# Performance work log

Measured on AMD Instinct MI355X. Metric: run time of the kernel, lower is better.

Reference implementation:

```python
import jax, jax.numpy as jnp
import numpy as np

E = 1024   # embed_dim
H = 16     # num_heads
D = E // H # head_dim
B = 2
S = 2048
YAT_EPS = 0.1


def setup_inputs() -> dict:
    key = jax.random.key(0)
    ks = jax.random.split(key, 5)
    w_scale = (6.0 / (E + E)) ** 0.5  # xavier_uniform bound
    def xavier(k):
        return jax.random.uniform(k, (E, E), jnp.float32, -w_scale, w_scale)
    return {
        "x": jax.random.normal(ks[0], (B, S, E), jnp.float32),
        "Wq": xavier(ks[1]), "bq": jnp.zeros((E,), jnp.float32),
        "Wk": xavier(ks[2]), "bk": jnp.zeros((E,), jnp.float32),
        "Wv": xavier(ks[3]), "bv": jnp.zeros((E,), jnp.float32),
        "Wo": xavier(ks[4]), "bo": jnp.zeros((E,), jnp.float32),
    }


def reference(x, Wq, bq, Wk, bk, Wv, bv, Wo, bo):
    b, s, _ = x.shape
    # Projections (Linear: x @ W + b, flax kernel layout [in, out])
    Q = x @ Wq + bq
    K = x @ Wk + bk
    V = x @ Wv + bv
    # [B, H, S, D]
    Q = Q.reshape(b, s, H, D).transpose(0, 2, 1, 3)
    K = K.reshape(b, s, H, D).transpose(0, 2, 1, 3)
    V = V.reshape(b, s, H, D).transpose(0, 2, 1, 3)
    # L2 normalize along head_dim
    Qn = Q / (jnp.linalg.norm(Q, axis=-1, keepdims=True) + 1e-8)
    Kn = K / (jnp.linalg.norm(K, axis=-1, keepdims=True) + 1e-8)
    # Yat kernel scores: (1 + <q,k>)^2 / (eps + (1 - <q,k>))
    dot = jnp.einsum("bhqd,bhkd->bhqk", Qn, Kn)
    scores = (1.0 + dot) ** 2 / (YAT_EPS + (1.0 - dot))
    # Sum-normalize (no softmax)
    attn = scores / (jnp.sum(scores, axis=-1, keepdims=True) + 1e-6)
    out = jnp.einsum("bhqk,bhkd->bhqd", attn, V)
    out = out.transpose(0, 2, 1, 3).reshape(b, s, E)
    return out @ Wo + bo
```

## Files before the change

### kernel.cpp

```cpp
#include <hip/hip_runtime.h>
#include <math.h>

#define EDIM 1024
#define NH   16
#define HD   64
#define BATCH 2
#define SEQ  2048
#define NROW (BATCH*SEQ)
#define YAT_EPS 0.1f

typedef _Float16 f16;
typedef _Float16 f16x8 __attribute__((ext_vector_type(8)));
typedef _Float16 f16x4 __attribute__((ext_vector_type(4)));
typedef __fp16   h16x2 __attribute__((ext_vector_type(2)));
typedef float    f32x4 __attribute__((ext_vector_type(4)));
typedef float    f32x2 __attribute__((ext_vector_type(2)));

static __device__ __forceinline__ int pk2(float a, float b) {
    union { h16x2 h; int i; } u;
    u.h = __builtin_amdgcn_cvt_pkrtz(a, b);
    return u.i;
}

static __device__ __forceinline__ f32x2 pk_fma(f32x2 a, f32x2 b, f32x2 c) {
    f32x2 d;
    asm("v_pk_fma_f32 %0, %1, %2, %3" : "=v"(d) : "v"(a), "v"(b), "v"(c));
    return d;
}
static __device__ __forceinline__ f32x2 pk_add(f32x2 a, f32x2 b) {
    f32x2 d;
    asm("v_pk_add_f32 %0, %1, %2" : "=v"(d) : "v"(a), "v"(b));
    return d;
}

__global__ __launch_bounds__(256)
void prep_kernel(const float* __restrict__ x, f16* __restrict__ xb,
                 const float* __restrict__ W0, const float* __restrict__ W1,
                 const float* __restrict__ W2, const float* __restrict__ W3,
                 f16* __restrict__ T0, f16* __restrict__ T1,
                 f16* __restrict__ T2, f16* __restrict__ T3)
{
    const int z = blockIdx.z;
    if (z == 4) {
        const int bid = blockIdx.y * 32 + blockIdx.x;
#pragma unroll
        for (int i = 0; i < 4; ++i) {
            const int off = bid * 4096 + i * 1024 + threadIdx.x * 4;
            const float4 v = *(const float4*)(x + off);
            union { int i2[2]; f16x4 h; } o;
            o.i2[0] = pk2(v.x, v.y);
            o.i2[1] = pk2(v.z, v.w);
            *(f16x4*)(xb + off) = o.h;
        }
        return;
    }
    const float* W = (z == 0) ? W0 : (z == 1) ? W1 : (z == 2) ? W2 : W3;
    f16*         Wt = (z == 0) ? T0 : (z == 1) ? T1 : (z == 2) ? T2 : T3;

    __shared__ float T[32][33];
    const int t = threadIdx.x;
    const int r = t >> 3, c4 = (t & 7) * 4;
    const int bi = blockIdx.x * 32, bj = blockIdx.y * 32;
    const float4 v = *(const float4*)(W + (size_t)(bi + r) * 1024 + bj + c4);
    T[r][c4 + 0] = v.x; T[r][c4 + 1] = v.y; T[r][c4 + 2] = v.z; T[r][c4 + 3] = v.w;
    __syncthreads();
    f16x4 o = {(f16)T[c4 + 0][r], (f16)T[c4 + 1][r], (f16)T[c4 + 2][r], (f16)T[c4 + 3][r]};
    *(f16x4*)(Wt + (size_t)(bj + r) * 1024 + bi + c4) = o;
}

template<int BM, int BN, int WM>
__global__ __launch_bounds__(WM * 128, 3)
void gemm_f16(const f16* __restrict__ A,
              const f16* __restrict__ B0, const f16* __restrict__ B1, const f16* __restrict__ B2,
              const float* __restrict__ bi0, const float* __restrict__ bi1, const float* __restrict__ bi2,
              void* __restrict__ o0, void* __restrict__ o1, void* __restrict__ o2,
              int e0, int e1, int e2)
{
    constexpr int NT    = WM * 128;
    constexpr int SR    = NT / 4;
    constexpr int ASL   = BM / SR;
    constexpr int BSL   = BN / SR;
    constexpr int ABUF  = BM * 32;
    constexpr int BBUF  = BN * 32;
    constexpr int WROWS = BM / WM;
    constexpr int MT    = WROWS / 16;
    constexpr int HALVES = BN / 128;
    constexpr int SCH    = 2048 / NT;
    __shared__ __align__(16) char lds[2 * (ABUF + BBUF) * 2];
    f16* As = (f16*)lds;
    f16* Bs = (f16*)lds + 2 * ABUF;

    const int z = blockIdx.z;
    const f16*   Bt   = (z == 0) ? B0  : (z == 1) ? B1  : B2;
    const float* bias = (z == 0) ? bi0 : (z == 1) ? bi1 : bi2;
    void*        Cout = (z == 0) ? o0  : (z == 1) ? o1  : o2;
    const int    epi  = (z == 0) ? e0  : (z == 1) ? e1  : e2;

    const int tid  = threadIdx.x;
    const int lane = tid & 63;
    const int w    = tid >> 6;
    const int cl   = lane & 15;
    const int quad = lane >> 4;
    const int wm = w % WM, wn = w / WM;
    const int bm = blockIdx.x * BM, bn = blockIdx.y * BN;
    const int wmoff = wm * WROWS;

    const int srow = tid >> 2;
    const int sc   = tid & 3;
    const int ssw  = (sc ^ (srow & 3)) * 8;
    const f16* gA = A  + (size_t)(bm + srow) * 1024 + sc * 8;
    const f16* gB = Bt + (size_t)(bn + srow) * 1024 + sc * 8;
    int lAo[ASL], lBo[BSL];
#pragma unroll
    for (int i = 0; i < ASL; ++i) lAo[i] = (srow + i * SR) * 32 + ssw;
#pragma unroll
    for (int i = 0; i < BSL; ++i) lBo[i] = (srow + i * SR) * 32 + ssw;

    f32x4 acc[MT][4];
#pragma unroll
    for (int i = 0; i < MT; ++i)
#pragma unroll
        for (int j = 0; j < 4; ++j) acc[i][j] = (f32x4){0.f, 0.f, 0.f, 0.f};

    f16x8 ra[ASL], rb[BSL];

#pragma unroll
    for (int i = 0; i < ASL; ++i) ra[i] = *(const f16x8*)(gA + (size_t)i * SR * 1024);
#pragma unroll
    for (int i = 0; i < BSL; ++i) rb[i] = *(const f16x8*)(gB + (size_t)i * SR * 1024);
#pragma unroll
    for (int i = 0; i < ASL; ++i) *(f16x8*)(As + lAo[i]) = ra[i];
#pragma unroll
    for (int i = 0; i < BSL; ++i) *(f16x8*)(Bs + lBo[i]) = rb[i];
#pragma unroll
    for (int i = 0; i < ASL; ++i) ra[i] = *(const f16x8*)(gA + (size_t)i * SR * 1024 + 32);
#pragma unroll
    for (int i = 0; i < BSL; ++i) rb[i] = *(const f16x8*)(gB + (size_t)i * SR * 1024 + 32);
    __syncthreads();

    const int fsw = (quad ^ (cl & 3)) * 8;

    for (int it = 0; it < 32; ++it) {
        const int buf = it & 1, nb = buf ^ 1;
        if (it < 31) {
#pragma unroll
            for (int i = 0; i < ASL; ++i) *(f16x8*)(As + nb * ABUF + lAo[i]) = ra[i];
#pragma unroll
            for (int i = 0; i < BSL; ++i) *(f16x8*)(Bs + nb * BBUF + lBo[i]) = rb[i];
        }
        if (it < 30) {
            const int kn = (it + 2) * 32;
#pragma unroll
            for (int i = 0; i < ASL; ++i) ra[i] = *(const f16x8*)(gA + (size_t)i * SR * 1024 + kn);
#pragma unroll
            for (int i = 0; i < BSL; ++i) rb[i] = *(const f16x8*)(gB + (size_t)i * SR * 1024 + kn);
        }
        f16x8 af[MT], bf[4];
#pragma unroll
        for (int mt = 0; mt < MT; ++mt)
            af[mt] = *(const f16x8*)(&As[buf * ABUF + (wmoff + mt * 16 + cl) * 32 + fsw]);
#pragma unroll
        for (int nt = 0; nt < 4; ++nt)
            bf[nt] = *(const f16x8*)(&Bs[buf * BBUF + (wn * 64 + nt * 16 + cl) * 32 + fsw]);
#pragma unroll
        for (int mt = 0; mt < MT; ++mt)
#pragma unroll
            for (int nt = 0; nt < 4; ++nt)
                acc[mt][nt] = __builtin_amdgcn_mfma_f32_16x16x32_f16(af[mt], bf[nt], acc[mt][nt], 0, 0, 0);
        __syncthreads();
    }

    float bcol[4];
#pragma unroll
    for (int nt = 0; nt < 4; ++nt) bcol[nt] = bias[bn + wn * 64 + nt * 16 + cl];
#pragma unroll
    for (int mt = 0; mt < MT; ++mt)
#pragma unroll
        for (int nt = 0; nt < 4; ++nt)
#pragma unroll
            for (int rg = 0; rg < 4; ++rg) acc[mt][nt][rg] += bcol[nt];

    const int b_idx = bm >> 11, sl0 = bm & (SEQ - 1), h0 = bn >> 6;

    if (epi == 0) {
        float* C = (float*)Cout;
#pragma unroll
        for (int mt = 0; mt < MT; ++mt)
#pragma unroll
            for (int rg = 0; rg < 4; ++rg) {
                const int row = bm + wmoff + mt * 16 + quad * 4 + rg;
#pragma unroll
                for (int nt = 0; nt < 4; ++nt)
                    C[(size_t)row * EDIM + bn + wn * 64 + nt * 16 + cl] = acc[mt][nt][rg];
            }
    } else if (epi == 1) {
        if constexpr (BM == 128) {
        f16* C = (f16*)Cout;
        f16* S = (f16*)lds;
#pragma unroll
        for (int h = 0; h < HALVES; ++h) {
            __syncthreads();
            if ((wn >> 1) == h) {
#pragma unroll
                for (int mt = 0; mt < MT; ++mt)
#pragma unroll
                    for (int rg = 0; rg < 4; ++rg) {
                        float ss = 0.f;
#pragma unroll
                        for (int nt = 0; nt < 4; ++nt) ss += acc[mt][nt][rg] * acc[mt][nt][rg];
                        ss += __shfl_xor(ss, 1); ss += __shfl_xor(ss, 2);
                        ss += __shfl_xor(ss, 4); ss += __shfl_xor(ss, 8);
                        const float inv = 1.0f / (sqrtf(ss) + 1e-8f);
                        const int row = wmoff + mt * 16 + quad * 4 + rg;
#pragma unroll
                        for (int nt = 0; nt < 4; ++nt) {
                            const int colh = (wn & 1) * 64 + nt * 16 + cl;
                            S[row * 128 + (((colh >> 3) ^ (row & 15)) * 8) + (colh & 7)] =
                                (f16)(acc[mt][nt][rg] * inv);
                        }
                    }
            }
            __syncthreads();
#pragma unroll
            for (int i = 0; i < SCH; ++i) {
                const int c = tid + i * NT;
                const int s = c >> 4, gi = c & 15;
                f16x8 v = *(const f16x8*)(&S[s * 128 + ((gi ^ (s & 15)) * 8)]);
                const int head = h0 + h * 2 + (gi >> 3), d8 = (gi & 7) * 8;
                *(f16x8*)(C + ((size_t)(b_idx * NH + head) * SEQ + sl0 + s) * HD + d8) = v;
            }
        }
        }
    } else {
        if constexpr (BM == 128) {
        f16* C = (f16*)Cout;
        f16* S = (f16*)lds;
#pragma unroll
        for (int h = 0; h < HALVES; ++h) {
            __syncthreads();
            if ((wn >> 1) == h) {
#pragma unroll
                for (int mt = 0; mt < MT; ++mt) {
                    const int s0 = wmoff + mt * 16 + quad * 4;
#pragma unroll
                    for (int nt = 0; nt < 4; ++nt) {
                        const int colh = (wn & 1) * 64 + nt * 16 + cl;
                        f16x4 o = {(f16)acc[mt][nt][0], (f16)acc[mt][nt][1],
                                   (f16)acc[mt][nt][2], (f16)acc[mt][nt][3]};
                        *(f16x4*)(&S[colh * 128 + (((s0 >> 3) ^ (colh & 15)) * 8) + (s0 & 7)]) = o;
                    }
                }
            }
            __syncthreads();
#pragma unroll
            for (int i = 0; i < SCH; ++i) {
                const int c = tid + i * NT;
                const int colh = c >> 4, gi = c & 15;
                f16x8 v = *(const f16x8*)(&S[colh * 128 + ((gi ^ (colh & 15)) * 8)]);
                const int head = h0 + h * 2 + (colh >> 6), d = colh & 63;
                *(f16x8*)(C + ((size_t)(b_idx * NH + head) * HD + d) * SEQ + sl0 + gi * 8) = v;
            }
        }
        }
    }
}

__global__ __launch_bounds__(512, 4)
void yat_attn(const f16* __restrict__ Qh, const f16* __restrict__ Kh,
              const f16* __restrict__ Vt, f16* __restrict__ AO)
{
    __shared__ __align__(16) char lds[49152];
    f16* Qs = (f16*)lds;
    f16* KB = (f16*)(lds + 16384);
    f16* VB = (f16*)(lds + 32768);

    const int tid  = threadIdx.x;
    const int lane = tid & 63;
    const int w    = tid >> 6;
    const int cl   = lane & 15;
    const int quad = lane >> 4;
    const int wm = w & 3;
    const int wk = w >> 2;
    const int q0 = blockIdx.x * 128;
    const int bh = blockIdx.y;

    const f16* Qg = Qh + (size_t)bh * SEQ * HD;
    const f16* Kg = Kh + (size_t)bh * SEQ * HD;
    const f16* Vg = Vt + (size_t)bh * HD * SEQ;

    const int rkv = tid >> 3;
    const int gkv = tid & 7;
    const f16* gK = Kg + (size_t)rkv * HD + gkv * 8;
    const f16* gV = Vg + (size_t)rkv * SEQ + gkv * 8;
    const int lkOff = rkv * 64 + ((gkv ^ (rkv & 7)) * 8);

    f16x8 kr = *(const f16x8*)(gK);
    f16x8 vr = *(const f16x8*)(gV);

#pragma unroll
    for (int i = 0; i < 2; ++i) {
        const int s0 = tid + i * 512;
        const int row = s0 >> 3, g = s0 & 7;
        f16x8 v = *(const f16x8*)(Qg + (size_t)(q0 + row) * HD + g * 8);
        *(f16x8*)(&Qs[row * 64 + ((g ^ (row & 7)) * 8)]) = v;
    }
    __syncthreads();
    f16x8 qf[2][2];
#pragma unroll
    for (int qt = 0; qt < 2; ++qt)
#pragma unroll
        for (int kb = 0; kb < 2; ++kb)
            qf[qt][kb] = *(const f16x8*)(&Qs[(wm * 32 + qt * 16 + cl) * 64 +
                                             ((kb * 4 + quad) ^ (cl & 7)) * 8]);

    f32x4 O[2][4];
    f32x2 rs_pk[2];
#pragma unroll
    for (int i = 0; i < 2; ++i) {
        rs_pk[i] = (f32x2){0.f, 0.f};
#pragma unroll
        for (int j = 0; j < 4; ++j) O[i][j] = (f32x4){0.f, 0.f, 0.f, 0.f};
    }

    const f32x2 c_m1  = {-1.0f, -1.0f};
    const f32x2 c_u0  = {1.0f + YAT_EPS, 1.0f + YAT_EPS};
    const f32x2 c_m42 = {-4.2f, -4.2f};
    const f32x2 c_441 = {4.41f, 4.41f};

    for (int t = 0; t < 32; ++t) {
        const int buf = t & 1;
        *(f16x8*)(&KB[buf * 4096 + lkOff]) = kr;
        *(f16x8*)(&VB[buf * 4096 + lkOff]) = vr;
        if (t < 31) {
            kr = *(const f16x8*)(gK + (size_t)(t + 1) * 64 * HD);
            vr = *(const f16x8*)(gV + (t + 1) * 64);
        }
        __syncthreads();

        const f16* Ks = KB + buf * 4096;
        const f16* Vs = VB + buf * 4096;

        f32x4 s[2][2];
#pragma unroll
        for (int kt = 0; kt < 2; ++kt)
#pragma unroll
            for (int qt = 0; qt < 2; ++qt) s[kt][qt] = (f32x4){0.f, 0.f, 0.f, 0.f};
        __builtin_amdgcn_s_setprio(1);
#pragma unroll
        for (int kb = 0; kb < 2; ++kb) {
            const int sw = ((kb * 4 + quad) ^ (cl & 7)) * 8;
            f16x8 af0 = *(const f16x8*)(&Ks[(wk * 32 +  0 + cl) * 64 + sw]);
            f16x8 af1 = *(const f16x8*)(&Ks[(wk * 32 + 16 + cl) * 64 + sw]);
#pragma unroll
            for (int qt = 0; qt < 2; ++qt) {
                s[0][qt] = __builtin_amdgcn_mfma_f32_16x16x32_f16(af0, qf[qt][kb], s[0][qt], 0, 0, 0);
                s[1][qt] = __builtin_amdgcn_mfma_f32_16x16x32_f16(af1, qf[qt][kb], s[1][qt], 0, 0, 0);
            }
        }
        __builtin_amdgcn_s_setprio(0);

        f16x4 pa16[2][2];
#pragma unroll
        for (int kt = 0; kt < 2; ++kt)
#pragma unroll
            for (int qt = 0; qt < 2; ++qt) {
                f32x2 d01 = {s[kt][qt][0], s[kt][qt][1]};
                f32x2 d23 = {s[kt][qt][2], s[kt][qt][3]};
                f32x2 u01 = pk_fma(d01, c_m1, c_u0);
                f32x2 u23 = pk_fma(d23, c_m1, c_u0);
                f32x2 r01 = {__builtin_amdgcn_rcpf(u01[0]), __builtin_amdgcn_rcpf(u01[1])};
                f32x2 r23 = {__builtin_amdgcn_rcpf(u23[0]), __builtin_amdgcn_rcpf(u23[1])};
                f32x2 p01 = pk_fma(c_441, r01, pk_add(u01, c_m42));
                f32x2 p23 = pk_fma(c_441, r23, pk_add(u23, c_m42));
                rs_pk[qt] = pk_add(rs_pk[qt], p01);
                rs_pk[qt] = pk_add(rs_pk[qt], p23);
                union { int i2[2]; f16x4 h; } pk_;
                pk_.i2[0] = pk2(p01[0], p01[1]);
                pk_.i2[1] = pk2(p23[0], p23[1]);
                pa16[kt][qt] = pk_.h;
            }

        __builtin_amdgcn_s_setprio(1);
#pragma unroll
        for (int kt = 0; kt < 2; ++kt)
#pragma unroll
            for (int dn = 0; dn < 4; ++dn) {
                const int row = dn * 16 + cl;
                const int g = wk * 4 + kt * 2 + (quad >> 1);
                f16x4 vb = *(const f16x4*)(&Vs[row * 64 + ((g ^ (row & 7)) * 8) + (quad & 1) * 4]);
#pragma unroll
                for (int qt = 0; qt < 2; ++qt)
                    O[qt][dn] = __builtin_amdgcn_mfma_f32_16x16x16f16(pa16[kt][qt], vb, O[qt][dn], 0, 0, 0);
            }
        __builtin_amdgcn_s_setprio(0);
    }

    __syncthreads();
    float* rs_s = (float*)lds;
    float* Ox   = (float*)(lds + 1024);

#pragma unroll
    for (int qt = 0; qt < 2; ++qt) {
        float t = rs_pk[qt][0] + rs_pk[qt][1];
        t += __shfl_xor(t, 16);
        t += __shfl_xor(t, 32);
        if (quad == 0) rs_s[wk * 128 + wm * 32 + qt * 16 + cl] = t;
    }
    if (wk == 1) {
#pragma unroll
        for (int qt = 0; qt < 2; ++qt)
#pragma unroll
            for (int dn = 0; dn < 4; ++dn)
#pragma unroll
                for (int rg = 0; rg < 4; ++rg)
                    Ox[(wm * 32 + qt * 16 + quad * 4 + rg) * 64 + dn * 16 + cl] = O[qt][dn][rg];
    }
    __syncthreads();
    if (wk == 0) {
        const int b = bh >> 4, h = bh & 15;
#pragma unroll
        for (int qt = 0; qt < 2; ++qt)
#pragma unroll
            for (int rg = 0; rg < 4; ++rg) {
                const int ql = wm * 32 + qt * 16 + quad * 4 + rg;
                const float tot = rs_s[ql] + rs_s[128 + ql];
                const float inv = 1.0f / (tot + 1e-6f);
                const size_t rowoff = ((size_t)b * SEQ + q0 + ql) * EDIM + h * 64;
#pragma unroll
                for (int dn = 0; dn < 4; ++dn)
                    AO[rowoff + dn * 16 + cl] =
                        (f16)((O[qt][dn][rg] + Ox[ql * 64 + dn * 16 + cl]) * inv);
            }
    }
}

extern "C" void kernel_launch(void* const* d_in, const int* in_sizes, int n_in,
                              void* d_out, int out_size, void* d_ws, size_t ws_size,
                              hipStream_t stream)
{
    const float* x  = (const float*)d_in[0];
    const float* Wq = (const float*)d_in[1];
    const float* bq = (const float*)d_in[2];
    const float* Wk = (const float*)d_in[3];
    const float* bk = (const float*)d_in[4];
    const float* Wv = (const float*)d_in[5];
    const float* bv = (const float*)d_in[6];
    const float* Wo = (const float*)d_in[7];
    const float* bo = (const float*)d_in[8];

    char* p = (char*)d_ws;
    f16* xb  = (f16*)p;                 p += (size_t)NROW * EDIM * 2;
    f16* Wqt = (f16*)p;                 p += (size_t)EDIM * EDIM * 2;
    f16* Wkt = (f16*)p;                 p += (size_t)EDIM * EDIM * 2;
    f16* Wvt = (f16*)p;                 p += (size_t)EDIM * EDIM * 2;
    f16* Wot = (f16*)p;                 p += (size_t)EDIM * EDIM * 2;
    f16* Qhb = (f16*)p;                 p += (size_t)NROW * EDIM * 2;
    f16* Khb = (f16*)p;                 p += (size_t)NROW * EDIM * 2;
    f16* Vtb = (f16*)p;                 p += (size_t)NROW * EDIM * 2;
    f16* AOb = (f16*)p;                 p += (size_t)NROW * EDIM * 2;

    prep_kernel<<<dim3(32, 32, 5), 256, 0, stream>>>(x, xb, Wq, Wk, Wv, Wo,
                                                     Wqt, Wkt, Wvt, Wot);

    gemm_f16<128, 128, 4><<<dim3(NROW / 128, EDIM / 128, 3), 512, 0, stream>>>(
        xb, Wqt, Wkt, Wvt, bq, bk, bv, Qhb, Khb, Vtb, 1, 1, 2);

    yat_attn<<<dim3(SEQ / 128, BATCH * NH), 512, 0, stream>>>(Qhb, Khb, Vtb, AOb);

    gemm_f16<64, 128, 2><<<dim3(NROW / 64, EDIM / 128, 1), 256, 0, stream>>>(
        AOb, Wot, Wot, Wot, bo, bo, bo, d_out, d_out, d_out, 0, 0, 0);
}
```

Before: 199.3 us.

## Use direct global-to-LDS loads in GEMM and drop packed-FP32 asm and setprio

```diff
diff --git a/kernel.cpp b/kernel.cpp
--- a/kernel.cpp
+++ b/kernel.cpp
@@ -14,7 +14,6 @@
 typedef _Float16 f16x4 __attribute__((ext_vector_type(4)));
 typedef __fp16   h16x2 __attribute__((ext_vector_type(2)));
 typedef float    f32x4 __attribute__((ext_vector_type(4)));
-typedef float    f32x2 __attribute__((ext_vector_type(2)));
 
 static __device__ __forceinline__ int pk2(float a, float b) {
     union { h16x2 h; int i; } u;
@@ -22,15 +21,11 @@
     return u.i;
 }
 
-static __device__ __forceinline__ f32x2 pk_fma(f32x2 a, f32x2 b, f32x2 c) {
-    f32x2 d;
-    asm("v_pk_fma_f32 %0, %1, %2, %3" : "=v"(d) : "v"(a), "v"(b), "v"(c));
-    return d;
-}
-static __device__ __forceinline__ f32x2 pk_add(f32x2 a, f32x2 b) {
-    f32x2 d;
-    asm("v_pk_add_f32 %0, %1, %2" : "=v"(d) : "v"(a), "v"(b));
-    return d;
+static __device__ __forceinline__ void gload16(const f16* g, f16* l) {
+    __builtin_amdgcn_global_load_lds(
+        (const __attribute__((address_space(1))) void*)g,
+        (__attribute__((address_space(3))) void*)l,
+        16, 0, 0);
 }
 
 __global__ __launch_bounds__(256)
@@ -107,14 +102,14 @@
 
     const int srow = tid >> 2;
     const int sc   = tid & 3;
-    const int ssw  = (sc ^ (srow & 3)) * 8;
-    const f16* gA = A  + (size_t)(bm + srow) * 1024 + sc * 8;
-    const f16* gB = Bt + (size_t)(bn + srow) * 1024 + sc * 8;
-    int lAo[ASL], lBo[BSL];
-#pragma unroll
-    for (int i = 0; i < ASL; ++i) lAo[i] = (srow + i * SR) * 32 + ssw;
-#pragma unroll
-    for (int i = 0; i < BSL; ++i) lBo[i] = (srow + i * SR) * 32 + ssw;
+    const int scg  = (sc ^ (srow & 3)) * 8;
+    const f16* gA = A  + (size_t)(bm + srow) * 1024 + scg;
+    const f16* gB = Bt + (size_t)(bn + srow) * 1024 + scg;
+    f16* lA[ASL]; f16* lB[BSL];
+#pragma unroll
+    for (int i = 0; i < ASL; ++i) lA[i] = As + (srow + i * SR) * 32 + sc * 8;
+#pragma unroll
+    for (int i = 0; i < BSL; ++i) lB[i] = Bs + (srow + i * SR) * 32 + sc * 8;
 
     f32x4 acc[MT][4];
 #pragma unroll
@@ -122,20 +117,10 @@
 #pragma unroll
         for (int j = 0; j < 4; ++j) acc[i][j] = (f32x4){0.f, 0.f, 0.f, 0.f};
 
-    f16x8 ra[ASL], rb[BSL];
-
-#pragma unroll
-    for (int i = 0; i < ASL; ++i) ra[i] = *(const f16x8*)(gA + (size_t)i * SR * 1024);
-#pragma unroll
-    for (int i = 0; i < BSL; ++i) rb[i] = *(const f16x8*)(gB + (size_t)i * SR * 1024);
-#pragma unroll
-    for (int i = 0; i < ASL; ++i) *(f16x8*)(As + lAo[i]) = ra[i];
-#pragma unroll
-    for (int i = 0; i < BSL; ++i) *(f16x8*)(Bs + lBo[i]) = rb[i];
-#pragma unroll
-    for (int i = 0; i < ASL; ++i) ra[i] = *(const f16x8*)(gA + (size_t)i * SR * 1024 + 32);
-#pragma unroll
-    for (int i = 0; i < BSL; ++i) rb[i] = *(const f16x8*)(gB + (size_t)i * SR * 1024 + 32);
+#pragma unroll
+    for (int i = 0; i < ASL; ++i) gload16(gA + (size_t)i * SR * 1024, lA[i]);
+#pragma unroll
+    for (int i = 0; i < BSL; ++i) gload16(gB + (size_t)i * SR * 1024, lB[i]);
     __syncthreads();
 
     const int fsw = (quad ^ (cl & 3)) * 8;
@@ -143,17 +128,13 @@
     for (int it = 0; it < 32; ++it) {
         const int buf = it & 1, nb = buf ^ 1;
         if (it < 31) {
-#pragma unroll
-            for (int i = 0; i < ASL; ++i) *(f16x8*)(As + nb * ABUF + lAo[i]) = ra[i];
-#pragma unroll
-            for (int i = 0; i < BSL; ++i) *(f16x8*)(Bs + nb * BBUF + lBo[i]) = rb[i];
-        }
-        if (it < 30) {
-            const int kn = (it + 2) * 32;
-#pragma unroll
-            for (int i = 0; i < ASL; ++i) ra[i] = *(const f16x8*)(gA + (size_t)i * SR * 1024 + kn);
-#pragma unroll
-            for (int i = 0; i < BSL; ++i) rb[i] = *(const f16x8*)(gB + (size_t)i * SR * 1024 + kn);
+            const int kn = (it + 1) * 32;
+#pragma unroll
+            for (int i = 0; i < ASL; ++i)
+                gload16(gA + (size_t)i * SR * 1024 + kn, lA[i] + nb * ABUF);
+#pragma unroll
+            for (int i = 0; i < BSL; ++i)
+                gload16(gB + (size_t)i * SR * 1024 + kn, lB[i] + nb * BBUF);
         }
         f16x8 af[MT], bf[4];
 #pragma unroll
@@ -314,18 +295,11 @@
                                              ((kb * 4 + quad) ^ (cl & 7)) * 8]);
 
     f32x4 O[2][4];
-    f32x2 rs_pk[2];
-#pragma unroll
-    for (int i = 0; i < 2; ++i) {
-        rs_pk[i] = (f32x2){0.f, 0.f};
+    float rs[2] = {0.f, 0.f};
+#pragma unroll
+    for (int i = 0; i < 2; ++i)
 #pragma unroll
         for (int j = 0; j < 4; ++j) O[i][j] = (f32x4){0.f, 0.f, 0.f, 0.f};
-    }
-
-    const f32x2 c_m1  = {-1.0f, -1.0f};
-    const f32x2 c_u0  = {1.0f + YAT_EPS, 1.0f + YAT_EPS};
-    const f32x2 c_m42 = {-4.2f, -4.2f};
-    const f32x2 c_441 = {4.41f, 4.41f};
 
     for (int t = 0; t < 32; ++t) {
         const int buf = t & 1;
@@ -345,7 +319,6 @@
         for (int kt = 0; kt < 2; ++kt)
 #pragma unroll
             for (int qt = 0; qt < 2; ++qt) s[kt][qt] = (f32x4){0.f, 0.f, 0.f, 0.f};
-        __builtin_amdgcn_s_setprio(1);
 #pragma unroll
         for (int kb = 0; kb < 2; ++kb) {
             const int sw = ((kb * 4 + quad) ^ (cl & 7)) * 8;
@@ -357,30 +330,25 @@
                 s[1][qt] = __builtin_amdgcn_mfma_f32_16x16x32_f16(af1, qf[qt][kb], s[1][qt], 0, 0, 0);
             }
         }
-        __builtin_amdgcn_s_setprio(0);
 
         f16x4 pa16[2][2];
 #pragma unroll
         for (int kt = 0; kt < 2; ++kt)
 #pragma unroll
             for (int qt = 0; qt < 2; ++qt) {
-                f32x2 d01 = {s[kt][qt][0], s[kt][qt][1]};
-                f32x2 d23 = {s[kt][qt][2], s[kt][qt][3]};
-                f32x2 u01 = pk_fma(d01, c_m1, c_u0);
-                f32x2 u23 = pk_fma(d23, c_m1, c_u0);
-                f32x2 r01 = {__builtin_amdgcn_rcpf(u01[0]), __builtin_amdgcn_rcpf(u01[1])};
-                f32x2 r23 = {__builtin_amdgcn_rcpf(u23[0]), __builtin_amdgcn_rcpf(u23[1])};
-                f32x2 p01 = pk_fma(c_441, r01, pk_add(u01, c_m42));
-                f32x2 p23 = pk_fma(c_441, r23, pk_add(u23, c_m42));
-                rs_pk[qt] = pk_add(rs_pk[qt], p01);
-                rs_pk[qt] = pk_add(rs_pk[qt], p23);
+                float p[4];
+#pragma unroll
+                for (int rg = 0; rg < 4; ++rg) {
+                    const float u = (1.0f + YAT_EPS) - s[kt][qt][rg];
+                    p[rg] = fmaf(4.41f, __builtin_amdgcn_rcpf(u), u - 4.2f);
+                    rs[qt] += p[rg];
+                }
                 union { int i2[2]; f16x4 h; } pk_;
-                pk_.i2[0] = pk2(p01[0], p01[1]);
-                pk_.i2[1] = pk2(p23[0], p23[1]);
+                pk_.i2[0] = pk2(p[0], p[1]);
+                pk_.i2[1] = pk2(p[2], p[3]);
                 pa16[kt][qt] = pk_.h;
             }
 
-        __builtin_amdgcn_s_setprio(1);
 #pragma unroll
         for (int kt = 0; kt < 2; ++kt)
 #pragma unroll
@@ -392,7 +360,6 @@
                 for (int qt = 0; qt < 2; ++qt)
                     O[qt][dn] = __builtin_amdgcn_mfma_f32_16x16x16f16(pa16[kt][qt], vb, O[qt][dn], 0, 0, 0);
             }
-        __builtin_amdgcn_s_setprio(0);
     }
 
     __syncthreads();
@@ -401,7 +368,7 @@
 
 #pragma unroll
     for (int qt = 0; qt < 2; ++qt) {
-        float t = rs_pk[qt][0] + rs_pk[qt][1];
+        float t = rs[qt];
         t += __shfl_xor(t, 16);
         t += __shfl_xor(t, 32);
         if (quad == 0) rs_s[wk * 128 + wm * 32 + qt * 16 + cl] = t;
```

Result: no change. 197.7 us, median of 2 (-0.8%).
